# Optimization experiments

Measured on AMD Instinct MI355X. Metric: run time of the kernel, lower is better.

Reference implementation:

```python
import jax, jax.numpy as jnp
import numpy as np
from jax import lax

BOS = 1


def setup_inputs() -> dict:
    key = jax.random.key(0)
    ks = jax.random.split(key, 12)
    B, T_ENC, D_ENC = 32, 800, 512   # D_ENC == att_odim
    E, H, V, ATT_H = 256, 512, 10000, 512
    s = 0.02
    return {
        "enc_pad": jax.random.normal(ks[0], (B, T_ENC, D_ENC), jnp.float32),
        "embedding": jax.random.normal(ks[1], (V, E), jnp.float32) * s,
        "W_ih": jax.random.normal(ks[2], (4 * H, E + D_ENC), jnp.float32) * s,
        "W_hh": jax.random.normal(ks[3], (4 * H, H), jnp.float32) * s,
        "b_ih": jnp.zeros((4 * H,), jnp.float32),
        "b_hh": jnp.zeros((4 * H,), jnp.float32),
        "W_enc": jax.random.normal(ks[4], (D_ENC, ATT_H), jnp.float32) * s,
        "W_dec": jax.random.normal(ks[5], (H, ATT_H), jnp.float32) * s,
        "v_att": jax.random.normal(ks[6], (ATT_H,), jnp.float32) * s,
        "W_out": jax.random.normal(ks[7], (V, H + D_ENC), jnp.float32) * s,
        "b_out": jnp.zeros((V,), jnp.float32),
        "enc_len": jax.random.randint(ks[8], (B,), 1, T_ENC + 1).astype(jnp.int32),
        "max_dec_timesteps": 100,
    }


def reference(enc_pad, embedding, W_ih, W_hh, b_ih, b_hh,
              W_enc, W_dec, v_att, W_out, b_out,
              enc_len, max_dec_timesteps):
    B, T, D = enc_pad.shape
    H = W_hh.shape[1]
    mask = jnp.arange(T)[None, :] < enc_len[:, None]          # [B,T]
    enc_proj = jnp.einsum('btd,da->bta', enc_pad, W_enc)       # precomputed enc keys
    NEG = jnp.float32(-1e30)

    def step(carry, _):
        dec_z, dec_c, c, pred = carry
        emb = jnp.take(embedding, pred, axis=0)                # [B,E]
        x = jnp.concatenate([emb, c], axis=-1)                 # cell_inp
        # torch.nn.LSTMCell gates
        gates = x @ W_ih.T + b_ih + dec_z @ W_hh.T + b_hh
        i, f, g, o = jnp.split(gates, 4, axis=-1)
        i, f, o = jax.nn.sigmoid(i), jax.nn.sigmoid(f), jax.nn.sigmoid(o)
        g = jnp.tanh(g)
        dec_c = f * dec_c + i * g
        dec_z = o * jnp.tanh(dec_c)
        # additive attention over encoder frames, masked by enc_len
        e = jnp.tanh(enc_proj + (dec_z @ W_dec)[:, None, :]) @ v_att  # [B,T]
        w = jax.nn.softmax(jnp.where(mask, e, NEG), axis=-1)
        c = jnp.einsum('bt,btd->bd', w, enc_pad)               # context, dim att_odim
        logit = jnp.concatenate([dec_z, c], axis=-1) @ W_out.T + b_out
        pred = jnp.argmax(logit, axis=-1)
        return (dec_z, dec_c, c, pred), (logit, pred, w)

    init = (jnp.zeros((B, H), enc_pad.dtype),
            jnp.zeros((B, H), enc_pad.dtype),
            jnp.zeros((B, D), enc_pad.dtype),
            jnp.full((B,), BOS, jnp.int32))
    _, (logits, preds, ws) = lax.scan(step, init, None, length=int(max_dec_timesteps))
    logits = jnp.swapaxes(logits, 0, 1)                        # [B,Tdec,V]
    preds = jnp.swapaxes(preds, 0, 1)                          # [B,Tdec]
    ws = jnp.swapaxes(ws, 0, 1)                                # [B,Tdec,Tenc]
    log_probs = jax.nn.log_softmax(logits, axis=2)
    ys_log_probs = jnp.take_along_axis(log_probs, preds[..., None], axis=2)[..., 0]
    return ys_log_probs, preds, ws
```

## Files before the change

### kernel.cpp

```cpp
#include <hip/hip_runtime.h>
#include <math.h>

#define B 32
#define T 800
#define E 256
#define H 512
#define V 10000
#define S 100

typedef float f4 __attribute__((ext_vector_type(4)));

#define OFF_ENCP 0
#define OFF_GP   (OFF_ENCP + B*T*512)
#define OFF_ZB   (OFF_GP + 4*B*2048)
#define OFF_DECC (OFF_ZB + B*512)
#define OFF_QV   (OFF_DECC + 2*B*512)
#define OFF_PB   (OFF_QV + B*512)
#define OFF_PSL  (OFF_PB + B*T)
#define OFF_CP   (OFF_PSL + B*16)
#define OFF_CTX  (OFF_CP + B*16*512)
#define OFF_KEY  (OFF_CTX + B*512)
#define OFF_ESUM (OFF_KEY + 128)

__device__ __forceinline__ float tanh_fast(float x) {
    float e = __expf(2.0f * x);
    return 1.0f - __fdividef(2.0f, e + 1.0f);
}

__global__ __launch_bounds__(256) void k_encproj(const float* Ap, const float* Wenc, float* outp) {
    __shared__ float Ast[16][68];
    __shared__ float Bs[16][68];
    int rb = blockIdx.x, cb = blockIdx.y;
    int tid = threadIdx.x;
    int tx = tid & 15, ty = tid >> 4;
    float acc[4][4] = {};
    for (int kb = 0; kb < 32; kb++) {
        #pragma unroll
        for (int i = 0; i < 4; i++) {
            int idx = tid + i*256;
            int r = idx >> 4, k = idx & 15;
            Ast[k][r] = Ap[(rb*64 + r)*512 + kb*16 + k];
        }
        #pragma unroll
        for (int i = 0; i < 4; i++) {
            int idx = tid + i*256;
            int k = idx >> 6, c = idx & 63;
            Bs[k][c] = Wenc[(kb*16 + k)*512 + cb*64 + c];
        }
        __syncthreads();
        #pragma unroll
        for (int kk = 0; kk < 16; kk++) {
            f4 a4 = *(const f4*)&Ast[kk][ty*4];
            f4 b4 = *(const f4*)&Bs[kk][tx*4];
            #pragma unroll
            for (int i = 0; i < 4; i++)
                #pragma unroll
                for (int j = 0; j < 4; j++)
                    acc[i][j] += a4[i] * b4[j];
        }
        __syncthreads();
    }
    #pragma unroll
    for (int i = 0; i < 4; i++)
        #pragma unroll
        for (int j = 0; j < 4; j++)
            outp[(rb*64 + ty*4 + i)*512 + cb*64 + tx*4 + j] = acc[i][j];
}

__global__ __launch_bounds__(512) void k_init(float* ws) {
    int idx = blockIdx.x*512 + threadIdx.x;
    ws[OFF_ZB + idx] = 0.f;
    ws[OFF_CTX + idx] = 0.f;
    ws[OFF_DECC + B*512 + idx] = 0.f;
    if (blockIdx.x == 0 && threadIdx.x < 32) {
        unsigned long long* key = (unsigned long long*)(ws + OFF_KEY);
        key[32 + threadIdx.x] = 0xFFFFFFFEull;
    }
}

__global__ __launch_bounds__(512) void ka_gates(const float* __restrict__ Wih,
    const float* __restrict__ Whh, const float* __restrict__ emb,
    float* __restrict__ ws, float* __restrict__ outp, int s) {
    __shared__ float xs[32*324];
    __shared__ float wt[32*324];
    __shared__ float part[8*32*33];
    __shared__ int preds[32];
    const int tid = threadIdx.x;
    const int jt = blockIdx.x, kq = blockIdx.y;
    const int p = s & 1;
    unsigned long long* keys = (unsigned long long*)(ws + OFF_KEY);
    float* esum = ws + OFF_ESUM;
    if (tid < 32) {
        unsigned long long k = keys[(p^1)*32 + tid];
        int pr = (int)(0xFFFFFFFFu - (unsigned)(k & 0xFFFFFFFFull));
        preds[tid] = pr;
        if (jt == 0 && kq == 0) {
            if (s > 0) {
                unsigned mu = (unsigned)(k >> 32);
                unsigned ou = (mu & 0x80000000u) ? (mu & 0x7FFFFFFFu) : ~mu;
                outp[tid*S + (s-1)] = __uint_as_float(ou) - logf(esum[(p^1)*32 + tid]);
                outp[B*S + tid*S + (s-1)] = (float)pr;
            }
            keys[p*32 + tid] = 0ull;
            esum[p*32 + tid] = 0.f;
        }
    }
    __syncthreads();
    const float* cbuf = ws + OFF_CTX;
    const float* zbuf = ws + OFF_ZB;
    #pragma unroll
    for (int i = 0; i < 5; i++) {
        int idx = tid + i*512;
        int b = idx / 80, c4 = idx - b*80;
        int k = kq*320 + c4*4;
        f4 v;
        if (k < 256)      v = *(const f4*)&emb[(size_t)preds[b]*E + k];
        else if (k < 768) v = *(const f4*)&cbuf[b*512 + (k-256)];
        else              v = *(const f4*)&zbuf[b*512 + (k-768)];
        *(f4*)&xs[b*324 + c4*4] = v;
    }
    #pragma unroll
    for (int i = 0; i < 5; i++) {
        int idx = tid + i*512;
        int r = idx / 80, c4 = idx - r*80;
        int kk = kq*320 + c4*4;
        int j = jt*32 + r;
        f4 v = (kk < 768) ? *(const f4*)&Wih[(size_t)j*768 + kk]
                          : *(const f4*)&Whh[(size_t)j*512 + (kk - 768)];
        *(f4*)&wt[r*324 + c4*4] = v;
    }
    __syncthreads();
    const int wid = tid >> 6, l = tid & 63;
    const int j0 = (l >> 3)*4, b0 = (l & 7)*4;
    const int ks0 = wid*40;
    float acc[4][4] = {};
    #pragma unroll 2
    for (int it = 0; it < 10; it++) {
        int k = ks0 + it*4;
        f4 w[4], x[4];
        #pragma unroll
        for (int i = 0; i < 4; i++) w[i] = *(const f4*)&wt[(j0 + i)*324 + k];
        #pragma unroll
        for (int j = 0; j < 4; j++) x[j] = *(const f4*)&xs[(b0 + j)*324 + k];
        #pragma unroll
        for (int i = 0; i < 4; i++)
            #pragma unroll
            for (int j = 0; j < 4; j++)
                acc[i][j] += w[i][0]*x[j][0] + w[i][1]*x[j][1]
                           + w[i][2]*x[j][2] + w[i][3]*x[j][3];
    }
    __syncthreads();
    #pragma unroll
    for (int i = 0; i < 4; i++)
        #pragma unroll
        for (int j = 0; j < 4; j++)
            part[wid*1056 + (j0 + i)*33 + (b0 + j)] = acc[i][j];
    __syncthreads();
    #pragma unroll
    for (int u = 0; u < 2; u++) {
        int o = tid + u*512;
        int j = o >> 5, b = o & 31;
        float g = 0.f;
        #pragma unroll
        for (int w2 = 0; w2 < 8; w2++) g += part[w2*1056 + j*33 + b];
        ws[OFF_GP + (kq*32 + b)*2048 + jt*32 + j] = g;
    }
}

__global__ __launch_bounds__(512) void kq_lstmq(const float* __restrict__ Wdec,
    const float* __restrict__ bih, const float* __restrict__ bhh,
    float* __restrict__ ws, int s) {
    __shared__ float zs[516];
    __shared__ float pq[4*516];
    const int tid = threadIdx.x, b = blockIdx.x;
    const int p = s & 1;
    const float* dold = ws + OFF_DECC + (p^1)*B*512;
    float* dnew = ws + OFF_DECC + p*B*512;
    {
        int h = tid;
        float gv[4];
        #pragma unroll
        for (int g = 0; g < 4; g++) {
            float sacc = bih[g*512 + h] + bhh[g*512 + h];
            #pragma unroll
            for (int kc = 0; kc < 4; kc++)
                sacc += ws[OFF_GP + (kc*32 + b)*2048 + g*512 + h];
            gv[g] = sacc;
        }
        float ig = 1.f/(1.f + expf(-gv[0]));
        float fg = 1.f/(1.f + expf(-gv[1]));
        float g2 = tanhf(gv[2]);
        float og = 1.f/(1.f + expf(-gv[3]));
        float c = fg*dold[b*512 + h] + ig*g2;
        dnew[b*512 + h] = c;
        float z = og*tanhf(c);
        zs[h] = z;
        ws[OFF_ZB + b*512 + h] = z;
    }
    __syncthreads();
    {
        const int aq = tid & 127, ks = tid >> 7;
        const int a0 = aq*4;
        f4 accq = {0.f, 0.f, 0.f, 0.f};
        #pragma unroll 4
        for (int kk = 0; kk < 128; kk += 4) {
            int k = ks*128 + kk;
            f4 z4 = *(const f4*)&zs[k];
            f4 w0 = *(const f4*)&Wdec[(size_t)(k+0)*512 + a0];
            f4 w1 = *(const f4*)&Wdec[(size_t)(k+1)*512 + a0];
            f4 w2 = *(const f4*)&Wdec[(size_t)(k+2)*512 + a0];
            f4 w3 = *(const f4*)&Wdec[(size_t)(k+3)*512 + a0];
            accq += z4[0]*w0 + z4[1]*w1 + z4[2]*w2 + z4[3]*w3;
        }
        *(f4*)&pq[ks*516 + a0] = accq;
    }
    __syncthreads();
    {
        int a = tid;
        float q = pq[a] + pq[516 + a] + pq[2*516 + a] + pq[3*516 + a];
        ws[OFF_QV + b*512 + a] = q;
    }
}

__global__ __launch_bounds__(512) void kb_ectx(const float* __restrict__ encpad,
    const float* __restrict__ vatt, const int* __restrict__ enclen,
    float* __restrict__ ws) {
    __shared__ float qs[512];
    __shared__ float vs[512];
    __shared__ float ep[50*132];
    __shared__ float p8[64][9];
    __shared__ float pl[52];
    const int tid = threadIdx.x;
    const int b = blockIdx.x >> 4, ts = blockIdx.x & 15;
    const int len = enclen[b];
    const int t0 = ts*50;
    const int nt = min(t0 + 50, len) - t0;
    qs[tid] = ws[OFF_QV + b*512 + tid];
    vs[tid] = vatt[tid];
    if (tid < 52) pl[tid] = 0.f;
    if (tid < 50) ws[OFF_PB + b*800 + t0 + tid] = 0.f;
    __syncthreads();
    const int c4 = tid & 127, tg = tid >> 7;
    const f4 q4 = *(const f4*)&qs[c4*4];
    const f4 vv = *(const f4*)&vs[c4*4];
    #pragma unroll
    for (int k = 0; k < 13; k++) {
        int tt = tg + 4*k;
        if (tt < nt) {
            f4 e4 = *(const f4*)&ws[OFF_ENCP + ((size_t)(b*800 + t0 + tt))*512 + c4*4];
            float sv = tanh_fast(e4[0]+q4[0])*vv[0] + tanh_fast(e4[1]+q4[1])*vv[1]
                     + tanh_fast(e4[2]+q4[2])*vv[2] + tanh_fast(e4[3]+q4[3])*vv[3];
            ep[tt*132 + c4] = sv;
        }
    }
    __syncthreads();
    {
        int t = tid >> 3, j = tid & 7;
        if (t < nt) {
            float sv = 0.f;
            #pragma unroll
            for (int m = 0; m < 16; m++) sv += ep[t*132 + j*16 + m];
            p8[t][j] = sv;
        }
    }
    __syncthreads();
    if (tid < nt) {
        float e = 0.f;
        #pragma unroll
        for (int j = 0; j < 8; j++) e += p8[tid][j];
        float pv = __expf(e);
        pl[tid] = pv;
        ws[OFF_PB + b*800 + t0 + tid] = pv;
    }
    __syncthreads();
    if (tid == 0) {
        float sacc = 0.f;
        for (int i = 0; i < 50; i++) sacc += pl[i];
        ws[OFF_PSL + b*16 + ts] = sacc;
    }
    f4 acc = {0.f, 0.f, 0.f, 0.f};
    #pragma unroll
    for (int k = 0; k < 13; k++) {
        int tt = tg + 4*k;
        if (tt < nt) {
            f4 e4 = *(const f4*)&encpad[((size_t)(b*800 + t0 + tt))*512 + c4*4];
            acc += pl[tt]*e4;
        }
    }
    __syncthreads();
    *(f4*)&ep[(tg*128 + c4)*4] = acc;
    __syncthreads();
    if (tid < 128) {
        f4 c = {0.f, 0.f, 0.f, 0.f};
        #pragma unroll
        for (int g = 0; g < 4; g++) c += *(const f4*)&ep[(g*128 + tid)*4];
        *(f4*)&ws[OFF_CP + (size_t)(b*16 + ts)*512 + tid*4] = c;
    }
}

__global__ __launch_bounds__(512) void kr_ctx(float* __restrict__ ws,
    float* __restrict__ outp, int s) {
    const int tid = threadIdx.x, b = blockIdx.x;
    __shared__ float invs;
    if (tid == 0) {
        float sacc = 0.f;
        #pragma unroll
        for (int i = 0; i < 16; i++) sacc += ws[OFF_PSL + b*16 + i];
        invs = 1.f / sacc;
    }
    __syncthreads();
    float inv = invs;
    {
        float c = 0.f;
        #pragma unroll
        for (int t2 = 0; t2 < 16; t2++) c += ws[OFF_CP + (size_t)(b*16 + t2)*512 + tid];
        ws[OFF_CTX + b*512 + tid] = c * inv;
    }
    float* wrow = outp + 2*B*S + (size_t)(b*S + s)*T;
    for (int t = tid; t < 800; t += 512)
        wrow[t] = ws[OFF_PB + b*800 + t] * inv;
}

__global__ __launch_bounds__(512) void kc_logits(const float* __restrict__ Wout,
    const float* __restrict__ bout, float* __restrict__ ws, int s) {
    __shared__ float sm[32*1028];
    const int tid = threadIdx.x, blk = blockIdx.x;
    const int p = s & 1;
    const int v0 = blk*40;
    #pragma unroll
    for (int i = 0; i < 8; i++) {
        int o = tid + i*512;
        int bb = o >> 7, qq = o & 127;
        *(f4*)&sm[bb*1028 + qq*4] = *(const f4*)&ws[OFF_ZB + bb*512 + qq*4];
        *(f4*)&sm[bb*1028 + 512 + qq*4] = *(const f4*)&ws[OFF_CTX + bb*512 + qq*4];
    }
    __syncthreads();
    const int wid = tid >> 6, l = tid & 63;
    const int vq = l & 7, bq2 = l >> 3;
    float acc[5][4] = {};
    const int kb = wid*128;
    const float* wbase = &Wout[(size_t)(v0 + vq*5)*1024 + kb];
    #pragma unroll 2
    for (int g = 0; g < 32; g++) {
        f4 w[5];
        #pragma unroll
        for (int i = 0; i < 5; i++) w[i] = *(const f4*)&wbase[i*1024 + g*4];
        #pragma unroll
        for (int j = 0; j < 4; j++) {
            f4 x4 = *(const f4*)&sm[(bq2+8*j)*1028 + kb + g*4];
            #pragma unroll
            for (int i = 0; i < 5; i++)
                acc[i][j] += w[i][0]*x4[0] + w[i][1]*x4[1] + w[i][2]*x4[2] + w[i][3]*x4[3];
        }
    }
    __syncthreads();
    #pragma unroll
    for (int i = 0; i < 5; i++)
        #pragma unroll
        for (int j = 0; j < 4; j++)
            sm[wid*1320 + (vq*5+i)*33 + (bq2+8*j)] = acc[i][j];
    __syncthreads();
    if (tid < 256) {
        int b = tid >> 3, u = tid & 7;
        float bmax = -3.0e38f; int bidx = 0; float bsum = 0.f;
        #pragma unroll
        for (int i = 0; i < 5; i++) {
            int r = u*5 + i;
            float lv = bout[v0 + r];
            #pragma unroll
            for (int w2 = 0; w2 < 8; w2++) lv += sm[w2*1320 + r*33 + b];
            bsum += __expf(lv);
            if (lv > bmax) { bmax = lv; bidx = v0 + r; }
        }
        #pragma unroll
        for (int off = 1; off < 8; off <<= 1) {
            float ov = __shfl_xor(bmax, off, 64);
            int oi = __shfl_xor(bidx, off, 64);
            float os = __shfl_xor(bsum, off, 64);
            bsum += os;
            if (ov > bmax || (ov == bmax && oi < bidx)) { bmax = ov; bidx = oi; }
        }
        if (u == 0) {
            unsigned mu = __float_as_uint(bmax);
            mu = (mu & 0x80000000u) ? ~mu : (mu | 0x80000000u);
            unsigned long long kk = ((unsigned long long)mu << 32)
                                  | (unsigned long long)(0xFFFFFFFFu - (unsigned)bidx);
            atomicMax((unsigned long long*)(ws + OFF_KEY) + p*32 + b, kk);
            atomicAdd(ws + OFF_ESUM + p*32 + b, bsum);
        }
    }
}

__global__ __launch_bounds__(64) void k_final(float* __restrict__ ws, float* __restrict__ outp) {
    int b = threadIdx.x;
    if (b < 32) {
        unsigned long long k = ((unsigned long long*)(ws + OFF_KEY))[32 + b];
        unsigned mu = (unsigned)(k >> 32);
        unsigned ou = (mu & 0x80000000u) ? (mu & 0x7FFFFFFFu) : ~mu;
        int pr = (int)(0xFFFFFFFFu - (unsigned)(k & 0xFFFFFFFFull));
        outp[b*S + 99] = __uint_as_float(ou) - logf(ws[OFF_ESUM + 32 + b]);
        outp[B*S + b*S + 99] = (float)pr;
    }
}

extern "C" void kernel_launch(void* const* d_in, const int* in_sizes, int n_in,
                              void* d_out, int out_size, void* d_ws, size_t ws_size,
                              hipStream_t stream) {
    (void)in_sizes; (void)n_in; (void)out_size; (void)ws_size;
    const float* encpad = (const float*)d_in[0];
    const float* emb    = (const float*)d_in[1];
    const float* Wih    = (const float*)d_in[2];
    const float* Whh    = (const float*)d_in[3];
    const float* bih    = (const float*)d_in[4];
    const float* bhh    = (const float*)d_in[5];
    const float* Wenc   = (const float*)d_in[6];
    const float* Wdec   = (const float*)d_in[7];
    const float* vatt   = (const float*)d_in[8];
    const float* Wout   = (const float*)d_in[9];
    const float* bout   = (const float*)d_in[10];
    const int*   enclen = (const int*)d_in[11];
    float* outp = (float*)d_out;
    float* ws   = (float*)d_ws;

    k_init<<<32, 512, 0, stream>>>(ws);
    k_encproj<<<dim3(400, 8), 256, 0, stream>>>(encpad, Wenc, ws + OFF_ENCP);

    for (int s = 0; s < S; s++) {
        ka_gates<<<dim3(64, 4), 512, 0, stream>>>(Wih, Whh, emb, ws, outp, s);
        kq_lstmq<<<32, 512, 0, stream>>>(Wdec, bih, bhh, ws, s);
        kb_ectx<<<512, 512, 0, stream>>>(encpad, vatt, enclen, ws);
        kr_ctx<<<32, 512, 0, stream>>>(ws, outp, s);
        kc_logits<<<250, 512, 0, stream>>>(Wout, bout, ws, s);
    }
    k_final<<<1, 64, 0, stream>>>(ws, outp);
}
```

Baseline: 9.454 ms.

## Fuse per-step decoder kernels into one persistent cooperative kernel with grid barriers

Replaces the 500 small per-step kernel launches with a single cooperative kernel of 256 blocks that runs all 100 decode steps. Stages are separated by a custom atomic grid barrier, and the LSTM cell state stays in a register instead of a global double buffer. The aim is to remove per-launch overhead and inter-kernel gaps. In exchange, the attention stage now runs with 256 blocks looping twice instead of 512 blocks, and each step pays for spin-wait barriers.

```diff
diff --git a/kernel.cpp b/kernel.cpp
--- a/kernel.cpp
+++ b/kernel.cpp
@@ -7,14 +7,17 @@
 #define H 512
 #define V 10000
 #define S 100
+#define NBLK 256
+#define NT 512
 
 typedef float f4 __attribute__((ext_vector_type(4)));
-
-#define OFF_ENCP 0
+#define AGT __HIP_MEMORY_SCOPE_AGENT
+
+#define OFF_BARS 0
+#define OFF_ENCP 512
 #define OFF_GP   (OFF_ENCP + B*T*512)
 #define OFF_ZB   (OFF_GP + 4*B*2048)
-#define OFF_DECC (OFF_ZB + B*512)
-#define OFF_QV   (OFF_DECC + 2*B*512)
+#define OFF_QV   (OFF_ZB + B*512)
 #define OFF_PB   (OFF_QV + B*512)
 #define OFF_PSL  (OFF_PB + B*T)
 #define OFF_CP   (OFF_PSL + B*16)
@@ -26,6 +29,30 @@
     float e = __expf(2.0f * x);
     return 1.0f - __fdividef(2.0f, e + 1.0f);
 }
+
+__device__ __forceinline__ void gsync(unsigned* cnt, unsigned* epoch, unsigned e) {
+    __syncthreads();
+    if (threadIdx.x == 0) {
+        __builtin_amdgcn_fence(__ATOMIC_RELEASE, "agent");
+        unsigned old = __hip_atomic_fetch_add(cnt, 1u, __ATOMIC_RELAXED, AGT);
+        if (old == NBLK - 1) {
+            __hip_atomic_store(cnt, 0u, __ATOMIC_RELAXED, AGT);
+            __hip_atomic_store(epoch, e, __ATOMIC_RELEASE, AGT);
+        } else {
+            while (__hip_atomic_load(epoch, __ATOMIC_RELAXED, AGT) < e)
+                __builtin_amdgcn_s_sleep(4);
+        }
+        __builtin_amdgcn_fence(__ATOMIC_ACQUIRE, "agent");
+    }
+    __syncthreads();
+}
+
+struct DecArgs {
+    const float* encpad; const float* emb; const float* Wih; const float* Whh;
+    const float* bih; const float* bhh; const float* Wdec; const float* vatt;
+    const float* Wout; const float* bout; const int* enclen;
+    float* outp; float* ws;
+};
 
 __global__ __launch_bounds__(256) void k_encproj(const float* Ap, const float* Wenc, float* outp) {
     __shared__ float Ast[16][68];
@@ -67,339 +94,351 @@
             outp[(rb*64 + ty*4 + i)*512 + cb*64 + tx*4 + j] = acc[i][j];
 }
 
-__global__ __launch_bounds__(512) void k_init(float* ws) {
-    int idx = blockIdx.x*512 + threadIdx.x;
-    ws[OFF_ZB + idx] = 0.f;
-    ws[OFF_CTX + idx] = 0.f;
-    ws[OFF_DECC + B*512 + idx] = 0.f;
-    if (blockIdx.x == 0 && threadIdx.x < 32) {
-        unsigned long long* key = (unsigned long long*)(ws + OFF_KEY);
-        key[32 + threadIdx.x] = 0xFFFFFFFEull;
+__global__ __launch_bounds__(NT) void coop_dec(DecArgs a) {
+    __shared__ float smem[32896];
+    const int tid = threadIdx.x;
+    const int blk = blockIdx.x;
+    unsigned* cnt   = (unsigned*)a.ws;
+    unsigned* epoch = (unsigned*)a.ws + 32;
+    float* GP  = a.ws + OFF_GP;
+    float* ZB  = a.ws + OFF_ZB;
+    float* QV  = a.ws + OFF_QV;
+    float* PB  = a.ws + OFF_PB;
+    float* PSL = a.ws + OFF_PSL;
+    float* CP  = a.ws + OFF_CP;
+    float* CTX = a.ws + OFF_CTX;
+    unsigned long long* KEYS = (unsigned long long*)(a.ws + OFF_KEY);
+    float* ESUM = a.ws + OFF_ESUM;
+    const float* encp = a.ws + OFF_ENCP;
+
+    float dc = 0.f;
+    unsigned ge = 1;
+
+    if (blk < 32) {
+        ZB[blk*512 + tid] = 0.f;
+        CTX[blk*512 + tid] = 0.f;
+        if (blk == 0 && tid < 32)
+            KEYS[32 + tid] = 0xFFFFFFFEull;
     }
-}
-
-__global__ __launch_bounds__(512) void ka_gates(const float* __restrict__ Wih,
-    const float* __restrict__ Whh, const float* __restrict__ emb,
-    float* __restrict__ ws, float* __restrict__ outp, int s) {
-    __shared__ float xs[32*324];
-    __shared__ float wt[32*324];
-    __shared__ float part[8*32*33];
-    __shared__ int preds[32];
-    const int tid = threadIdx.x;
-    const int jt = blockIdx.x, kq = blockIdx.y;
-    const int p = s & 1;
-    unsigned long long* keys = (unsigned long long*)(ws + OFF_KEY);
-    float* esum = ws + OFF_ESUM;
-    if (tid < 32) {
-        unsigned long long k = keys[(p^1)*32 + tid];
-        int pr = (int)(0xFFFFFFFFu - (unsigned)(k & 0xFFFFFFFFull));
-        preds[tid] = pr;
-        if (jt == 0 && kq == 0) {
-            if (s > 0) {
-                unsigned mu = (unsigned)(k >> 32);
-                unsigned ou = (mu & 0x80000000u) ? (mu & 0x7FFFFFFFu) : ~mu;
-                outp[tid*S + (s-1)] = __uint_as_float(ou) - logf(esum[(p^1)*32 + tid]);
-                outp[B*S + tid*S + (s-1)] = (float)pr;
-            }
-            keys[p*32 + tid] = 0ull;
-            esum[p*32 + tid] = 0.f;
-        }
+    gsync(cnt, epoch, ge++);
+
+    #pragma unroll 1
+    for (int s = 0; s < S; s++) {
+        const int par = s & 1;
+
+        {
+            const int jt = blk >> 2, kq = blk & 3;
+            float* xs = smem;
+            float* wt = smem + 10368;
+            float* part = smem + 20736;
+            int* preds = (int*)(smem + 29184);
+            if (tid < 32) {
+                unsigned long long k = __hip_atomic_load(&KEYS[(par^1)*32 + tid],
+                                                         __ATOMIC_RELAXED, AGT);
+                int pr = (int)(0xFFFFFFFFu - (unsigned)(k & 0xFFFFFFFFull));
+                preds[tid] = pr;
+                if (blk == 0) {
+                    if (s > 0) {
+                        unsigned mu = (unsigned)(k >> 32);
+                        unsigned ou = (mu & 0x80000000u) ? (mu & 0x7FFFFFFFu) : ~mu;
+                        a.outp[tid*S + (s-1)] = __uint_as_float(ou)
+                                              - logf(ESUM[(par^1)*32 + tid]);
+                        a.outp[B*S + tid*S + (s-1)] = (float)pr;
+                    }
+                    KEYS[par*32 + tid] = 0ull;
+                    ESUM[par*32 + tid] = 0.f;
+                }
+            }
+            __syncthreads();
+            #pragma unroll
+            for (int i = 0; i < 5; i++) {
+                int idx = tid + i*512;
+                int b = idx / 80, c4 = idx - b*80;
+                int k = kq*320 + c4*4;
+                f4 v;
+                if (k < 256)      v = *(const f4*)&a.emb[(size_t)preds[b]*E + k];
+                else if (k < 768) v = *(const f4*)&CTX[b*512 + (k-256)];
+                else              v = *(const f4*)&ZB[b*512 + (k-768)];
+                *(f4*)&xs[b*324 + c4*4] = v;
+            }
+            #pragma unroll
+            for (int i = 0; i < 5; i++) {
+                int idx = tid + i*512;
+                int r = idx / 80, c4 = idx - r*80;
+                int kk = kq*320 + c4*4;
+                int j = jt*32 + r;
+                f4 v = (kk < 768) ? *(const f4*)&a.Wih[(size_t)j*768 + kk]
+                                  : *(const f4*)&a.Whh[(size_t)j*512 + (kk - 768)];
+                *(f4*)&wt[r*324 + c4*4] = v;
+            }
+            __syncthreads();
+            const int wid = tid >> 6, l = tid & 63;
+            const int j0 = (l >> 3)*4, b0 = (l & 7)*4;
+            const int ks0 = wid*40;
+            float acc[4][4] = {};
+            #pragma unroll 2
+            for (int it = 0; it < 10; it++) {
+                int k = ks0 + it*4;
+                f4 w[4], x[4];
+                #pragma unroll
+                for (int i = 0; i < 4; i++) w[i] = *(const f4*)&wt[(j0 + i)*324 + k];
+                #pragma unroll
+                for (int j = 0; j < 4; j++) x[j] = *(const f4*)&xs[(b0 + j)*324 + k];
+                #pragma unroll
+                for (int i = 0; i < 4; i++)
+                    #pragma unroll
+                    for (int j = 0; j < 4; j++)
+                        acc[i][j] += w[i][0]*x[j][0] + w[i][1]*x[j][1]
+                                   + w[i][2]*x[j][2] + w[i][3]*x[j][3];
+            }
+            __syncthreads();
+            #pragma unroll
+            for (int i = 0; i < 4; i++)
+                #pragma unroll
+                for (int j = 0; j < 4; j++)
+                    part[wid*1056 + (j0 + i)*33 + (b0 + j)] = acc[i][j];
+            __syncthreads();
+            #pragma unroll
+            for (int u = 0; u < 2; u++) {
+                int o = tid + u*512;
+                int j = o >> 5, b = o & 31;
+                float g = 0.f;
+                #pragma unroll
+                for (int w2 = 0; w2 < 8; w2++) g += part[w2*1056 + j*33 + b];
+                GP[(kq*32 + b)*2048 + jt*32 + j] = g;
+            }
+        }
+        gsync(cnt, epoch, ge++);
+
+        if (blk < 32) {
+            const int b = blk;
+            float* zs = smem;
+            float* pq = smem + 516;
+            {
+                int h = tid;
+                float gv[4];
+                #pragma unroll
+                for (int g = 0; g < 4; g++) {
+                    float sacc = a.bih[g*512 + h] + a.bhh[g*512 + h];
+                    #pragma unroll
+                    for (int kc = 0; kc < 4; kc++)
+                        sacc += GP[(kc*32 + b)*2048 + g*512 + h];
+                    gv[g] = sacc;
+                }
+                float ig = 1.f/(1.f + expf(-gv[0]));
+                float fg = 1.f/(1.f + expf(-gv[1]));
+                float g2 = tanhf(gv[2]);
+                float og = 1.f/(1.f + expf(-gv[3]));
+                float c = fg*dc + ig*g2;
+                dc = c;
+                float z = og*tanhf(c);
+                zs[h] = z;
+                ZB[b*512 + h] = z;
+            }
+            __syncthreads();
+            {
+                const int aq = tid & 127, ks = tid >> 7;
+                const int a0 = aq*4;
+                f4 accq = {0.f, 0.f, 0.f, 0.f};
+                #pragma unroll 4
+                for (int kk = 0; kk < 128; kk += 4) {
+                    int k = ks*128 + kk;
+                    f4 z4 = *(const f4*)&zs[k];
+                    f4 w0 = *(const f4*)&a.Wdec[(size_t)(k+0)*512 + a0];
+                    f4 w1 = *(const f4*)&a.Wdec[(size_t)(k+1)*512 + a0];
+                    f4 w2 = *(const f4*)&a.Wdec[(size_t)(k+2)*512 + a0];
+                    f4 w3 = *(const f4*)&a.Wdec[(size_t)(k+3)*512 + a0];
+                    accq += z4[0]*w0 + z4[1]*w1 + z4[2]*w2 + z4[3]*w3;
+                }
+                *(f4*)&pq[ks*516 + a0] = accq;
+            }
+            __syncthreads();
+            {
+                int a2 = tid;
+                QV[b*512 + a2] = pq[a2] + pq[516 + a2] + pq[2*516 + a2] + pq[3*516 + a2];
+            }
+        }
+        gsync(cnt, epoch, ge++);
+
+        #pragma unroll 1
+        for (int it2 = 0; it2 < 2; it2++) {
+            const int vb = blk + it2*256;
+            const int b = vb >> 4, ts = vb & 15;
+            const int len = a.enclen[b];
+            const int t0 = ts*50;
+            int ntt = len - t0; if (ntt < 0) ntt = 0; if (ntt > 50) ntt = 50;
+            const int nt = ntt;
+            float* qs = smem;
+            float* vs = smem + 512;
+            float* ep = smem + 1024;
+            float* p8 = smem + 7624;
+            float* pl = smem + 8200;
+            __syncthreads();
+            qs[tid] = QV[b*512 + tid];
+            vs[tid] = a.vatt[tid];
+            __syncthreads();
+            const int c4 = tid & 127, tg = tid >> 7;
+            const f4 q4 = *(const f4*)&qs[c4*4];
+            const f4 vv = *(const f4*)&vs[c4*4];
+            #pragma unroll
+            for (int k = 0; k < 13; k++) {
+                int tt = tg + 4*k;
+                if (tt < nt) {
+                    f4 e4 = *(const f4*)&encp[((size_t)(b*800 + t0 + tt))*512 + c4*4];
+                    float sv = tanh_fast(e4[0]+q4[0])*vv[0] + tanh_fast(e4[1]+q4[1])*vv[1]
+                             + tanh_fast(e4[2]+q4[2])*vv[2] + tanh_fast(e4[3]+q4[3])*vv[3];
+                    ep[tt*132 + c4] = sv;
+                }
+            }
+            __syncthreads();
+            {
+                int t = tid >> 3, j = tid & 7;
+                if (t < nt) {
+                    float sv = 0.f;
+                    #pragma unroll
+                    for (int m = 0; m < 16; m++) sv += ep[t*132 + j*16 + m];
+                    p8[t*9 + j] = sv;
+                }
+            }
+            __syncthreads();
+            if (tid < 50) {
+                float pv = 0.f;
+                if (tid < nt) {
+                    float e = 0.f;
+                    #pragma unroll
+                    for (int j = 0; j < 8; j++) e += p8[tid*9 + j];
+                    pv = __expf(e);
+                }
+                pl[tid] = pv;
+                PB[b*800 + t0 + tid] = pv;
+            }
+            __syncthreads();
+            if (tid == 0) {
+                float sacc = 0.f;
+                for (int i = 0; i < 50; i++) sacc += pl[i];
+                PSL[b*16 + ts] = sacc;
+            }
+            f4 acc = {0.f, 0.f, 0.f, 0.f};
+            #pragma unroll
+            for (int k = 0; k < 13; k++) {
+                int tt = tg + 4*k;
+                if (tt < nt) {
+                    f4 e4 = *(const f4*)&a.encpad[((size_t)(b*800 + t0 + tt))*512 + c4*4];
+                    acc += pl[tt]*e4;
+                }
+            }
+            __syncthreads();
+            *(f4*)&ep[(tg*128 + c4)*4] = acc;
+            __syncthreads();
+            if (tid < 128) {
+                f4 c = {0.f, 0.f, 0.f, 0.f};
+                #pragma unroll
+                for (int g = 0; g < 4; g++) c += *(const f4*)&ep[(g*128 + tid)*4];
+                *(f4*)&CP[(size_t)(b*16 + ts)*512 + tid*4] = c;
+            }
+        }
+        gsync(cnt, epoch, ge++);
+
+        if (blk < 32) {
+            const int b = blk;
+            if (tid == 0) {
+                float sacc = 0.f;
+                #pragma unroll
+                for (int i = 0; i < 16; i++) sacc += PSL[b*16 + i];
+                smem[0] = 1.f / sacc;
+            }
+            __syncthreads();
+            float inv = smem[0];
+            {
+                float c = 0.f;
+                #pragma unroll
+                for (int t2 = 0; t2 < 16; t2++)
+                    c += CP[(size_t)(b*16 + t2)*512 + tid];
+                CTX[b*512 + tid] = c * inv;
+            }
+            float* wrow = a.outp + 2*B*S + (size_t)(b*S + s)*T;
+            for (int t = tid; t < 800; t += 512)
+                wrow[t] = PB[b*800 + t] * inv;
+        }
+        gsync(cnt, epoch, ge++);
+
+        if (blk < 250) {
+            float* sm = smem;
+            const int v0 = blk*40;
+            #pragma unroll
+            for (int i = 0; i < 8; i++) {
+                int o = tid + i*512;
+                int bb = o >> 7, qq = o & 127;
+                *(f4*)&sm[bb*1028 + qq*4] = *(const f4*)&ZB[bb*512 + qq*4];
+                *(f4*)&sm[bb*1028 + 512 + qq*4] = *(const f4*)&CTX[bb*512 + qq*4];
+            }
+            __syncthreads();
+            const int wid = tid >> 6, l = tid & 63;
+            const int vq = l & 7, bq2 = l >> 3;
+            float acc[5][4] = {};
+            const int kb = wid*128;
+            const float* wbase = &a.Wout[(size_t)(v0 + vq*5)*1024 + kb];
+            #pragma unroll 2
+            for (int g = 0; g < 32; g++) {
+                f4 w[5];
+                #pragma unroll
+                for (int i = 0; i < 5; i++) w[i] = *(const f4*)&wbase[i*1024 + g*4];
+                #pragma unroll
+                for (int j = 0; j < 4; j++) {
+                    f4 x4 = *(const f4*)&sm[(bq2+8*j)*1028 + kb + g*4];
+                    #pragma unroll
+                    for (int i = 0; i < 5; i++)
+                        acc[i][j] += w[i][0]*x4[0] + w[i][1]*x4[1]
+                                   + w[i][2]*x4[2] + w[i][3]*x4[3];
+                }
+            }
+            __syncthreads();
+            #pragma unroll
+            for (int i = 0; i < 5; i++)
+                #pragma unroll
+                for (int j = 0; j < 4; j++)
+                    sm[wid*1320 + (vq*5+i)*33 + (bq2+8*j)] = acc[i][j];
+            __syncthreads();
+            if (tid < 256) {
+                int b = tid >> 3, u = tid & 7;
+                float bmax = -3.0e38f; int bidx = 0; float bsum = 0.f;
+                #pragma unroll
+                for (int i = 0; i < 5; i++) {
+                    int r = u*5 + i;
+                    float lv = a.bout[v0 + r];
+                    #pragma unroll
+                    for (int w2 = 0; w2 < 8; w2++) lv += sm[w2*1320 + r*33 + b];
+                    bsum += __expf(lv);
+                    if (lv > bmax) { bmax = lv; bidx = v0 + r; }
+                }
+                #pragma unroll
+                for (int off = 1; off < 8; off <<= 1) {
+                    float ov = __shfl_xor(bmax, off, 64);
+                    int oi = __shfl_xor(bidx, off, 64);
+                    float os = __shfl_xor(bsum, off, 64);
+                    bsum += os;
+                    if (ov > bmax || (ov == bmax && oi < bidx)) { bmax = ov; bidx = oi; }
+                }
+                if (u == 0) {
+                    unsigned mu = __float_as_uint(bmax);
+                    mu = (mu & 0x80000000u) ? ~mu : (mu | 0x80000000u);
+                    unsigned long long kk = ((unsigned long long)mu << 32)
+                                          | (unsigned long long)(0xFFFFFFFFu - (unsigned)bidx);
+                    atomicMax(&KEYS[par*32 + b], kk);
+                    atomicAdd(&ESUM[par*32 + b], bsum);
+                }
+            }
+        }
+        gsync(cnt, epoch, ge++);
     }
-    __syncthreads();
-    const float* cbuf = ws + OFF_CTX;
-    const float* zbuf = ws + OFF_ZB;
-    #pragma unroll
-    for (int i = 0; i < 5; i++) {
-        int idx = tid + i*512;
-        int b = idx / 80, c4 = idx - b*80;
-        int k = kq*320 + c4*4;
-        f4 v;
-        if (k < 256)      v = *(const f4*)&emb[(size_t)preds[b]*E + k];
-        else if (k < 768) v = *(const f4*)&cbuf[b*512 + (k-256)];
-        else              v = *(const f4*)&zbuf[b*512 + (k-768)];
-        *(f4*)&xs[b*324 + c4*4] = v;
-    }
-    #pragma unroll
-    for (int i = 0; i < 5; i++) {
-        int idx = tid + i*512;
-        int r = idx / 80, c4 = idx - r*80;
-        int kk = kq*320 + c4*4;
-        int j = jt*32 + r;
-        f4 v = (kk < 768) ? *(const f4*)&Wih[(size_t)j*768 + kk]
-                          : *(const f4*)&Whh[(size_t)j*512 + (kk - 768)];
-        *(f4*)&wt[r*324 + c4*4] = v;
-    }
-    __syncthreads();
-    const int wid = tid >> 6, l = tid & 63;
-    const int j0 = (l >> 3)*4, b0 = (l & 7)*4;
-    const int ks0 = wid*40;
-    float acc[4][4] = {};
-    #pragma unroll 2
-    for (int it = 0; it < 10; it++) {
-        int k = ks0 + it*4;
-        f4 w[4], x[4];
-        #pragma unroll
-        for (int i = 0; i < 4; i++) w[i] = *(const f4*)&wt[(j0 + i)*324 + k];
-        #pragma unroll
-        for (int j = 0; j < 4; j++) x[j] = *(const f4*)&xs[(b0 + j)*324 + k];
-        #pragma unroll
-        for (int i = 0; i < 4; i++)
-            #pragma unroll
-            for (int j = 0; j < 4; j++)
-                acc[i][j] += w[i][0]*x[j][0] + w[i][1]*x[j][1]
-                           + w[i][2]*x[j][2] + w[i][3]*x[j][3];
-    }
-    __syncthreads();
-    #pragma unroll
-    for (int i = 0; i < 4; i++)
-        #pragma unroll
-        for (int j = 0; j < 4; j++)
-            part[wid*1056 + (j0 + i)*33 + (b0 + j)] = acc[i][j];
-    __syncthreads();
-    #pragma unroll
-    for (int u = 0; u < 2; u++) {
-        int o = tid + u*512;
-        int j = o >> 5, b = o & 31;
-        float g = 0.f;
-        #pragma unroll
-        for (int w2 = 0; w2 < 8; w2++) g += part[w2*1056 + j*33 + b];
-        ws[OFF_GP + (kq*32 + b)*2048 + jt*32 + j] = g;
-    }
-}
-
-__global__ __launch_bounds__(512) void kq_lstmq(const float* __restrict__ Wdec,
-    const float* __restrict__ bih, const float* __restrict__ bhh,
-    float* __restrict__ ws, int s) {
-    __shared__ float zs[516];
-    __shared__ float pq[4*516];
-    const int tid = threadIdx.x, b = blockIdx.x;
-    const int p = s & 1;
-    const float* dold = ws + OFF_DECC + (p^1)*B*512;
-    float* dnew = ws + OFF_DECC + p*B*512;
-    {
-        int h = tid;
-        float gv[4];
-        #pragma unroll
-        for (int g = 0; g < 4; g++) {
-            float sacc = bih[g*512 + h] + bhh[g*512 + h];
-            #pragma unroll
-            for (int kc = 0; kc < 4; kc++)
-                sacc += ws[OFF_GP + (kc*32 + b)*2048 + g*512 + h];
-            gv[g] = sacc;
-        }
-        float ig = 1.f/(1.f + expf(-gv[0]));
-        float fg = 1.f/(1.f + expf(-gv[1]));
-        float g2 = tanhf(gv[2]);
-        float og = 1.f/(1.f + expf(-gv[3]));
-        float c = fg*dold[b*512 + h] + ig*g2;
-        dnew[b*512 + h] = c;
-        float z = og*tanhf(c);
-        zs[h] = z;
-        ws[OFF_ZB + b*512 + h] = z;
-    }
-    __syncthreads();
-    {
-        const int aq = tid & 127, ks = tid >> 7;
-        const int a0 = aq*4;
-        f4 accq = {0.f, 0.f, 0.f, 0.f};
-        #pragma unroll 4
-        for (int kk = 0; kk < 128; kk += 4) {
-            int k = ks*128 + kk;
-            f4 z4 = *(const f4*)&zs[k];
-            f4 w0 = *(const f4*)&Wdec[(size_t)(k+0)*512 + a0];
-            f4 w1 = *(const f4*)&Wdec[(size_t)(k+1)*512 + a0];
-            f4 w2 = *(const f4*)&Wdec[(size_t)(k+2)*512 + a0];
-            f4 w3 = *(const f4*)&Wdec[(size_t)(k+3)*512 + a0];
-            accq += z4[0]*w0 + z4[1]*w1 + z4[2]*w2 + z4[3]*w3;
-        }
-        *(f4*)&pq[ks*516 + a0] = accq;
-    }
-    __syncthreads();
-    {
-        int a = tid;
-        float q = pq[a] + pq[516 + a] + pq[2*516 + a] + pq[3*516 + a];
-        ws[OFF_QV + b*512 + a] = q;
-    }
-}
-
-__global__ __launch_bounds__(512) void kb_ectx(const float* __restrict__ encpad,
-    const float* __restrict__ vatt, const int* __restrict__ enclen,
-    float* __restrict__ ws) {
-    __shared__ float qs[512];
-    __shared__ float vs[512];
-    __shared__ float ep[50*132];
-    __shared__ float p8[64][9];
-    __shared__ float pl[52];
-    const int tid = threadIdx.x;
-    const int b = blockIdx.x >> 4, ts = blockIdx.x & 15;
-    const int len = enclen[b];
-    const int t0 = ts*50;
-    const int nt = min(t0 + 50, len) - t0;
-    qs[tid] = ws[OFF_QV + b*512 + tid];
-    vs[tid] = vatt[tid];
-    if (tid < 52) pl[tid] = 0.f;
-    if (tid < 50) ws[OFF_PB + b*800 + t0 + tid] = 0.f;
-    __syncthreads();
-    const int c4 = tid & 127, tg = tid >> 7;
-    const f4 q4 = *(const f4*)&qs[c4*4];
-    const f4 vv = *(const f4*)&vs[c4*4];
-    #pragma unroll
-    for (int k = 0; k < 13; k++) {
-        int tt = tg + 4*k;
-        if (tt < nt) {
-            f4 e4 = *(const f4*)&ws[OFF_ENCP + ((size_t)(b*800 + t0 + tt))*512 + c4*4];
-            float sv = tanh_fast(e4[0]+q4[0])*vv[0] + tanh_fast(e4[1]+q4[1])*vv[1]
-                     + tanh_fast(e4[2]+q4[2])*vv[2] + tanh_fast(e4[3]+q4[3])*vv[3];
-            ep[tt*132 + c4] = sv;
-        }
-    }
-    __syncthreads();
-    {
-        int t = tid >> 3, j = tid & 7;
-        if (t < nt) {
-            float sv = 0.f;
-            #pragma unroll
-            for (int m = 0; m < 16; m++) sv += ep[t*132 + j*16 + m];
-            p8[t][j] = sv;
-        }
-    }
-    __syncthreads();
-    if (tid < nt) {
-        float e = 0.f;
-        #pragma unroll
-        for (int j = 0; j < 8; j++) e += p8[tid][j];
-        float pv = __expf(e);
-        pl[tid] = pv;
-        ws[OFF_PB + b*800 + t0 + tid] = pv;
-    }
-    __syncthreads();
-    if (tid == 0) {
-        float sacc = 0.f;
-        for (int i = 0; i < 50; i++) sacc += pl[i];
-        ws[OFF_PSL + b*16 + ts] = sacc;
-    }
-    f4 acc = {0.f, 0.f, 0.f, 0.f};
-    #pragma unroll
-    for (int k = 0; k < 13; k++) {
-        int tt = tg + 4*k;
-        if (tt < nt) {
-            f4 e4 = *(const f4*)&encpad[((size_t)(b*800 + t0 + tt))*512 + c4*4];
-            acc += pl[tt]*e4;
-        }
-    }
-    __syncthreads();
-    *(f4*)&ep[(tg*128 + c4)*4] = acc;
-    __syncthreads();
-    if (tid < 128) {
-        f4 c = {0.f, 0.f, 0.f, 0.f};
-        #pragma unroll
-        for (int g = 0; g < 4; g++) c += *(const f4*)&ep[(g*128 + tid)*4];
-        *(f4*)&ws[OFF_CP + (size_t)(b*16 + ts)*512 + tid*4] = c;
-    }
-}
-
-__global__ __launch_bounds__(512) void kr_ctx(float* __restrict__ ws,
-    float* __restrict__ outp, int s) {
-    const int tid = threadIdx.x, b = blockIdx.x;
-    __shared__ float invs;
-    if (tid == 0) {
-        float sacc = 0.f;
-        #pragma unroll
-        for (int i = 0; i < 16; i++) sacc += ws[OFF_PSL + b*16 + i];
-        invs = 1.f / sacc;
-    }
-    __syncthreads();
-    float inv = invs;
-    {
-        float c = 0.f;
-        #pragma unroll
-        for (int t2 = 0; t2 < 16; t2++) c += ws[OFF_CP + (size_t)(b*16 + t2)*512 + tid];
-        ws[OFF_CTX + b*512 + tid] = c * inv;
-    }
-    float* wrow = outp + 2*B*S + (size_t)(b*S + s)*T;
-    for (int t = tid; t < 800; t += 512)
-        wrow[t] = ws[OFF_PB + b*800 + t] * inv;
-}
-
-__global__ __launch_bounds__(512) void kc_logits(const float* __restrict__ Wout,
-    const float* __restrict__ bout, float* __restrict__ ws, int s) {
-    __shared__ float sm[32*1028];
-    const int tid = threadIdx.x, blk = blockIdx.x;
-    const int p = s & 1;
-    const int v0 = blk*40;
-    #pragma unroll
-    for (int i = 0; i < 8; i++) {
-        int o = tid + i*512;
-        int bb = o >> 7, qq = o & 127;
-        *(f4*)&sm[bb*1028 + qq*4] = *(const f4*)&ws[OFF_ZB + bb*512 + qq*4];
-        *(f4*)&sm[bb*1028 + 512 + qq*4] = *(const f4*)&ws[OFF_CTX + bb*512 + qq*4];
-    }
-    __syncthreads();
-    const int wid = tid >> 6, l = tid & 63;
-    const int vq = l & 7, bq2 = l >> 3;
-    float acc[5][4] = {};
-    const int kb = wid*128;
-    const float* wbase = &Wout[(size_t)(v0 + vq*5)*1024 + kb];
-    #pragma unroll 2
-    for (int g = 0; g < 32; g++) {
-        f4 w[5];
-        #pragma unroll
-        for (int i = 0; i < 5; i++) w[i] = *(const f4*)&wbase[i*1024 + g*4];
-        #pragma unroll
-        for (int j = 0; j < 4; j++) {
-            f4 x4 = *(const f4*)&sm[(bq2+8*j)*1028 + kb + g*4];
-            #pragma unroll
-            for (int i = 0; i < 5; i++)
-                acc[i][j] += w[i][0]*x4[0] + w[i][1]*x4[1] + w[i][2]*x4[2] + w[i][3]*x4[3];
-        }
-    }
-    __syncthreads();
-    #pragma unroll
-    for (int i = 0; i < 5; i++)
-        #pragma unroll
-        for (int j = 0; j < 4; j++)
-            sm[wid*1320 + (vq*5+i)*33 + (bq2+8*j)] = acc[i][j];
-    __syncthreads();
-    if (tid < 256) {
-        int b = tid >> 3, u = tid & 7;
-        float bmax = -3.0e38f; int bidx = 0; float bsum = 0.f;
-        #pragma unroll
-        for (int i = 0; i < 5; i++) {
-            int r = u*5 + i;
-            float lv = bout[v0 + r];
-            #pragma unroll
-            for (int w2 = 0; w2 < 8; w2++) lv += sm[w2*1320 + r*33 + b];
-            bsum += __expf(lv);
-            if (lv > bmax) { bmax = lv; bidx = v0 + r; }
-        }
-        #pragma unroll
-        for (int off = 1; off < 8; off <<= 1) {
-            float ov = __shfl_xor(bmax, off, 64);
-            int oi = __shfl_xor(bidx, off, 64);
-            float os = __shfl_xor(bsum, off, 64);
-            bsum += os;
-            if (ov > bmax || (ov == bmax && oi < bidx)) { bmax = ov; bidx = oi; }
-        }
-        if (u == 0) {
-            unsigned mu = __float_as_uint(bmax);
-            mu = (mu & 0x80000000u) ? ~mu : (mu | 0x80000000u);
-            unsigned long long kk = ((unsigned long long)mu << 32)
-                                  | (unsigned long long)(0xFFFFFFFFu - (unsigned)bidx);
-            atomicMax((unsigned long long*)(ws + OFF_KEY) + p*32 + b, kk);
-            atomicAdd(ws + OFF_ESUM + p*32 + b, bsum);
-        }
-    }
-}
-
-__global__ __launch_bounds__(64) void k_final(float* __restrict__ ws, float* __restrict__ outp) {
-    int b = threadIdx.x;
-    if (b < 32) {
-        unsigned long long k = ((unsigned long long*)(ws + OFF_KEY))[32 + b];
+
+    if (blk == 0 && tid < 32) {
+        unsigned long long k = __hip_atomic_load(&KEYS[32 + tid], __ATOMIC_RELAXED, AGT);
         unsigned mu = (unsigned)(k >> 32);
         unsigned ou = (mu & 0x80000000u) ? (mu & 0x7FFFFFFFu) : ~mu;
         int pr = (int)(0xFFFFFFFFu - (unsigned)(k & 0xFFFFFFFFull));
-        outp[b*S + 99] = __uint_as_float(ou) - logf(ws[OFF_ESUM + 32 + b]);
-        outp[B*S + b*S + 99] = (float)pr;
+        a.outp[tid*S + 99] = __uint_as_float(ou) - logf(ESUM[32 + tid]);
+        a.outp[B*S + tid*S + 99] = (float)pr;
     }
 }
 
@@ -422,15 +461,13 @@
     float* outp = (float*)d_out;
     float* ws   = (float*)d_ws;
 
-    k_init<<<32, 512, 0, stream>>>(ws);
+    hipMemsetAsync(d_ws, 0, 2048, stream);
+
     k_encproj<<<dim3(400, 8), 256, 0, stream>>>(encpad, Wenc, ws + OFF_ENCP);
 
-    for (int s = 0; s < S; s++) {
-        ka_gates<<<dim3(64, 4), 512, 0, stream>>>(Wih, Whh, emb, ws, outp, s);
-        kq_lstmq<<<32, 512, 0, stream>>>(Wdec, bih, bhh, ws, s);
-        kb_ectx<<<512, 512, 0, stream>>>(encpad, vatt, enclen, ws);
-        kr_ctx<<<32, 512, 0, stream>>>(ws, outp, s);
-        kc_logits<<<250, 512, 0, stream>>>(Wout, bout, ws, s);
-    }
-    k_final<<<1, 64, 0, stream>>>(ws, outp);
+    DecArgs args = { encpad, emb, Wih, Whh, bih, bhh, Wdec, vatt, Wout, bout,
+                     enclen, outp, ws };
+    void* kp[] = { &args };
+    hipLaunchCooperativeKernel((const void*)coop_dec, dim3(NBLK), dim3(NT),
+                               kp, 0, stream);
 }
```

After: 13.76 ms. 1.46x slower.

## Drop LDS staging of weights in gates and activations in logits, double logits grid

Applied to the files above, without the earlier changes.

The gates kernel no longer copies its W_ih/W_hh tile into shared memory and instead reads weights straight from global memory inside the dot-product loop. The logits kernel drops the 128KB shared buffer of z/context activations and reads them directly from global, with a smaller partial-sum buffer. It now covers 20 vocab rows per block over 500 blocks instead of 40 over 250. The aim is lower LDS use and higher occupancy on these memory-bound matvecs, at the cost of more global and L2 traffic for the activations.

```diff
diff --git a/kernel.cpp b/kernel.cpp
--- a/kernel.cpp
+++ b/kernel.cpp
@@ -82,7 +82,6 @@
     const float* __restrict__ Whh, const float* __restrict__ emb,
     float* __restrict__ ws, float* __restrict__ outp, int s) {
     __shared__ float xs[32*324];
-    __shared__ float wt[32*324];
     __shared__ float part[8*32*33];
     __shared__ int preds[32];
     const int tid = threadIdx.x;
@@ -119,16 +118,6 @@
         else              v = *(const f4*)&zbuf[b*512 + (k-768)];
         *(f4*)&xs[b*324 + c4*4] = v;
     }
-    #pragma unroll
-    for (int i = 0; i < 5; i++) {
-        int idx = tid + i*512;
-        int r = idx / 80, c4 = idx - r*80;
-        int kk = kq*320 + c4*4;
-        int j = jt*32 + r;
-        f4 v = (kk < 768) ? *(const f4*)&Wih[(size_t)j*768 + kk]
-                          : *(const f4*)&Whh[(size_t)j*512 + (kk - 768)];
-        *(f4*)&wt[r*324 + c4*4] = v;
-    }
     __syncthreads();
     const int wid = tid >> 6, l = tid & 63;
     const int j0 = (l >> 3)*4, b0 = (l & 7)*4;
@@ -137,9 +126,18 @@
     #pragma unroll 2
     for (int it = 0; it < 10; it++) {
         int k = ks0 + it*4;
-        f4 w[4], x[4];
-        #pragma unroll
-        for (int i = 0; i < 4; i++) w[i] = *(const f4*)&wt[(j0 + i)*324 + k];
+        int kk = kq*320 + k;
+        f4 w[4];
+        if (kk < 768) {
+            #pragma unroll
+            for (int i = 0; i < 4; i++)
+                w[i] = *(const f4*)&Wih[(size_t)(jt*32 + j0 + i)*768 + kk];
+        } else {
+            #pragma unroll
+            for (int i = 0; i < 4; i++)
+                w[i] = *(const f4*)&Whh[(size_t)(jt*32 + j0 + i)*512 + (kk - 768)];
+        }
+        f4 x[4];
         #pragma unroll
         for (int j = 0; j < 4; j++) x[j] = *(const f4*)&xs[(b0 + j)*324 + k];
         #pragma unroll
@@ -323,57 +321,52 @@
 
 __global__ __launch_bounds__(512) void kc_logits(const float* __restrict__ Wout,
     const float* __restrict__ bout, float* __restrict__ ws, int s) {
-    __shared__ float sm[32*1028];
+    __shared__ float part[8*660];
     const int tid = threadIdx.x, blk = blockIdx.x;
     const int p = s & 1;
-    const int v0 = blk*40;
-    #pragma unroll
-    for (int i = 0; i < 8; i++) {
-        int o = tid + i*512;
-        int bb = o >> 7, qq = o & 127;
-        *(f4*)&sm[bb*1028 + qq*4] = *(const f4*)&ws[OFF_ZB + bb*512 + qq*4];
-        *(f4*)&sm[bb*1028 + 512 + qq*4] = *(const f4*)&ws[OFF_CTX + bb*512 + qq*4];
-    }
-    __syncthreads();
+    const int v0 = blk*20;
     const int wid = tid >> 6, l = tid & 63;
-    const int vq = l & 7, bq2 = l >> 3;
-    float acc[5][4] = {};
+    const int vq = l & 3, bq2 = l >> 2;
+    float acc[5][2] = {};
     const int kb = wid*128;
     const float* wbase = &Wout[(size_t)(v0 + vq*5)*1024 + kb];
+    const float* xz = ws + OFF_ZB;
+    const float* xc = ws + OFF_CTX;
     #pragma unroll 2
     for (int g = 0; g < 32; g++) {
         f4 w[5];
         #pragma unroll
         for (int i = 0; i < 5; i++) w[i] = *(const f4*)&wbase[i*1024 + g*4];
         #pragma unroll
-        for (int j = 0; j < 4; j++) {
-            f4 x4 = *(const f4*)&sm[(bq2+8*j)*1028 + kb + g*4];
+        for (int j = 0; j < 2; j++) {
+            int bb = bq2 + 16*j;
+            f4 x4 = (kb < 512) ? *(const f4*)&xz[bb*512 + kb + g*4]
+                               : *(const f4*)&xc[bb*512 + (kb - 512) + g*4];
             #pragma unroll
             for (int i = 0; i < 5; i++)
                 acc[i][j] += w[i][0]*x4[0] + w[i][1]*x4[1] + w[i][2]*x4[2] + w[i][3]*x4[3];
         }
     }
-    __syncthreads();
     #pragma unroll
     for (int i = 0; i < 5; i++)
         #pragma unroll
-        for (int j = 0; j < 4; j++)
-            sm[wid*1320 + (vq*5+i)*33 + (bq2+8*j)] = acc[i][j];
-    __syncthreads();
-    if (tid < 256) {
-        int b = tid >> 3, u = tid & 7;
+        for (int j = 0; j < 2; j++)
+            part[wid*660 + (vq*5 + i)*33 + (bq2 + 16*j)] = acc[i][j];
+    __syncthreads();
+    if (tid < 128) {
+        int b = tid >> 2, u = tid & 3;
         float bmax = -3.0e38f; int bidx = 0; float bsum = 0.f;
         #pragma unroll
         for (int i = 0; i < 5; i++) {
             int r = u*5 + i;
             float lv = bout[v0 + r];
             #pragma unroll
-            for (int w2 = 0; w2 < 8; w2++) lv += sm[w2*1320 + r*33 + b];
+            for (int w2 = 0; w2 < 8; w2++) lv += part[w2*660 + r*33 + b];
             bsum += __expf(lv);
             if (lv > bmax) { bmax = lv; bidx = v0 + r; }
         }
         #pragma unroll
-        for (int off = 1; off < 8; off <<= 1) {
+        for (int off = 1; off < 4; off <<= 1) {
             float ov = __shfl_xor(bmax, off, 64);
             int oi = __shfl_xor(bidx, off, 64);
             float os = __shfl_xor(bsum, off, 64);
@@ -430,7 +423,7 @@
         kq_lstmq<<<32, 512, 0, stream>>>(Wdec, bih, bhh, ws, s);
         kb_ectx<<<512, 512, 0, stream>>>(encpad, vatt, enclen, ws);
         kr_ctx<<<32, 512, 0, stream>>>(ws, outp, s);
-        kc_logits<<<250, 512, 0, stream>>>(Wout, bout, ws, s);
+        kc_logits<<<500, 512, 0, stream>>>(Wout, bout, ws, s);
     }
     k_final<<<1, 64, 0, stream>>>(ws, outp);
 }
```

After: 13.22 ms. 1.4x slower.
